# Kernel optimization log

Hardware: AMD Instinct MI355X
Metric: run time of the kernel (lower is better)

The kernel has to match this reference:

```python
import jax, jax.numpy as jnp
import numpy as np

ALPHA = 0.2  # LeakyReLU negative slope
NEG_INF = -9e15  # matches torch's -9000000000000000.0


def setup_inputs() -> dict:
    key = jax.random.key(0)
    k1, k2, k3, k4 = jax.random.split(key, 4)
    B, T, N, F_in, D = 4, 32, 512, 128, 128
    h = jax.random.normal(k1, (B, T, N, F_in), dtype=jnp.float32)
    adj = jax.random.randint(k2, (N, N), 0, 2, dtype=jnp.int32)
    # params: W ~ Linear(in_dim, out_dim, bias=False); a ~ Linear(2*out_dim, 1, bias=False)
    W = jax.random.normal(k3, (F_in, D), dtype=jnp.float32) * 0.05
    a = jax.random.normal(k4, (2 * D,), dtype=jnp.float32) * 0.05
    return {"h": h, "adj": adj, "W": W, "a": a}


def reference(h, adj, W, a):
    # h: (B,T,N,F_in), adj: (N,N), W: (F_in,D), a: (2D,)
    D = W.shape[1]
    Wh = jnp.einsum('btnf,fd->btnd', h, W)  # (B,T,N,D)
    # a . [Wh_i ; Wh_j] == a_src . Wh_i + a_dst . Wh_j -- avoids (N,N,2D) concat
    a_src, a_dst = a[:D], a[D:]
    e_src = Wh @ a_src  # (B,T,N)
    e_dst = Wh @ a_dst  # (B,T,N)
    e = jax.nn.leaky_relu(e_src[..., :, None] + e_dst[..., None, :], ALPHA)  # (B,T,N,N)
    e = jnp.where(adj > 0, e, jnp.float32(NEG_INF))
    attention = jax.nn.softmax(e, axis=-1)  # dropout is identity at eval
    h_prime = jnp.einsum('btij,btjd->btid', attention, Wh)  # (B,T,N,D)
    return h_prime
```

## Files before the change

kernel.cpp:

```cpp
#include <hip/hip_runtime.h>
#include <math.h>

typedef __attribute__((ext_vector_type(8))) short bf16x8;
typedef __attribute__((ext_vector_type(4))) float f32x4;

#define MFMA(a, b, c) __builtin_amdgcn_mfma_f32_16x16x32_bf16(a, b, c, 0, 0, 0)

constexpr int GN = 128;
constexpr int NN = 512;
constexpr int FD = 128;
#define LOG2E 1.4426950408889634f

__device__ inline unsigned rne_top16(float x) {
    unsigned u = __float_as_uint(x);
    return u + 0x7fffu + ((u >> 16) & 1u);
}
__device__ inline unsigned pack_top16(unsigned e1, unsigned e0) {
    return __builtin_amdgcn_perm(e1, e0, 0x07060302u);
}

__global__ __launch_bounds__(1024) void gat_fused_kernel(
    const float* __restrict__ h, const float* __restrict__ a,
    const int* __restrict__ adj, const float* __restrict__ W,
    float* __restrict__ out)
{
    __shared__ __attribute__((aligned(16))) unsigned short sWh[65536];
    __shared__ __attribute__((aligned(16))) float sEsrc[NN];
    __shared__ __attribute__((aligned(16))) float sEdst[NN];

    const int bid = blockIdx.x;
    const int xcd = bid & 7, slot = bid >> 3;
    const int g  = xcd * 16 + (slot >> 1);
    const int hf = slot & 1;
    const int t = threadIdx.x, lane = t & 63, w = t >> 6;
    const int l15 = lane & 15, q8 = (lane >> 4) * 8;
    const float* hg = h + (size_t)g * NN * FD;

    #pragma unroll
    for (int rep = 0; rep < 2; ++rep) {
        const int p = rep * 1024 + t;
        const int lanep = p & 63, cn2 = p >> 6;
        const int kbase = (cn2 >> 3) * 32 + ((lanep >> 4) & 3) * 8;
        const int d = (cn2 & 7) * 16 + (lanep & 15);
        unsigned hi[8], lo[8];
        #pragma unroll
        for (int idx = 0; idx < 8; ++idx) {
            const float wv = W[(kbase + idx) * FD + d];
            const unsigned u = __float_as_uint(wv);
            hi[idx] = u;
            lo[idx] = rne_top16(wv - __uint_as_float(u & 0xffff0000u));
        }
        uint4 H4, L4;
        H4.x = pack_top16(hi[1], hi[0]); H4.y = pack_top16(hi[3], hi[2]);
        H4.z = pack_top16(hi[5], hi[4]); H4.w = pack_top16(hi[7], hi[6]);
        L4.x = pack_top16(lo[1], lo[0]); L4.y = pack_top16(lo[3], lo[2]);
        L4.z = pack_top16(lo[5], lo[4]); L4.w = pack_top16(lo[7], lo[6]);
        *(uint4*)&sWh[32768 + p * 8] = H4;
        *(uint4*)&sWh[49152 + p * 8] = L4;
    }
    __syncthreads();

    f32x4 acc1[2][8];
    #pragma unroll
    for (int mt = 0; mt < 2; ++mt)
        #pragma unroll
        for (int nb = 0; nb < 8; ++nb) acc1[mt][nb] = (f32x4){0.f, 0.f, 0.f, 0.f};

    #pragma unroll
    for (int kk = 0; kk < 4; ++kk) {
        float4 hv[4];
        #pragma unroll
        for (int mt = 0; mt < 2; ++mt) {
            const float* src = hg + (size_t)(w * 32 + mt * 16 + l15) * FD
                             + kk * 32 + q8;
            hv[2 * mt]     = *(const float4*)src;
            hv[2 * mt + 1] = *(const float4*)(src + 4);
        }
        bf16x8 ah[2], al[2];
        #pragma unroll
        for (int mt = 0; mt < 2; ++mt) {
            const float4 f0 = hv[2 * mt], f1 = hv[2 * mt + 1];
            const float xs[8] = {f0.x, f0.y, f0.z, f0.w, f1.x, f1.y, f1.z, f1.w};
            union { bf16x8 v; unsigned u[4]; } H, L;
            #pragma unroll
            for (int j = 0; j < 4; ++j) {
                const unsigned e0 = __float_as_uint(xs[2 * j]);
                const unsigned e1 = __float_as_uint(xs[2 * j + 1]);
                H.u[j] = pack_top16(e1, e0);
                const unsigned l0 = rne_top16(xs[2*j]   - __uint_as_float(e0 & 0xffff0000u));
                const unsigned l1 = rne_top16(xs[2*j+1] - __uint_as_float(e1 & 0xffff0000u));
                L.u[j] = pack_top16(l1, l0);
            }
            ah[mt] = H.v; al[mt] = L.v;
        }
        #pragma unroll
        for (int nb = 0; nb < 8; ++nb) {
            const bf16x8 bh = *(const bf16x8*)&sWh[32768 + ((kk * 8 + nb) * 64 + lane) * 8];
            const bf16x8 bl = *(const bf16x8*)&sWh[49152 + ((kk * 8 + nb) * 64 + lane) * 8];
            #pragma unroll
            for (int mt = 0; mt < 2; ++mt) {
                acc1[mt][nb] = MFMA(al[mt], bh, acc1[mt][nb]);
                acc1[mt][nb] = MFMA(ah[mt], bl, acc1[mt][nb]);
                acc1[mt][nb] = MFMA(ah[mt], bh, acc1[mt][nb]);
            }
        }
    }

    {
        float av[8], bv[8];
        #pragma unroll
        for (int nb = 0; nb < 8; ++nb) {
            av[nb] = a[nb * 16 + l15];
            bv[nb] = a[FD + nb * 16 + l15];
        }
        #pragma unroll
        for (int mt = 0; mt < 2; ++mt)
            #pragma unroll
            for (int r = 0; r < 4; ++r) {
                float ps = 0.f, pd = 0.f;
                #pragma unroll
                for (int nb = 0; nb < 8; ++nb) {
                    ps += acc1[mt][nb][r] * av[nb];
                    pd += acc1[mt][nb][r] * bv[nb];
                }
                #pragma unroll
                for (int off = 1; off <= 8; off <<= 1) {
                    ps += __shfl_xor(ps, off);
                    pd += __shfl_xor(pd, off);
                }
                if (l15 == 0) {
                    const int row = w * 32 + mt * 16 + (lane >> 4) * 4 + r;
                    sEsrc[row] = ps * LOG2E;
                    sEdst[row] = pd * LOG2E;
                }
            }
    }
    __syncthreads();

    {
        const int ib = 4 * ((lane >> 4) & 1);
        #pragma unroll
        for (int mt = 0; mt < 2; ++mt) {
            const int lp2 = l15 + 16 * (mt * 2 + (lane >> 5));
            #pragma unroll
            for (int nb = 0; nb < 8; ++nb) {
                const int off = ((w * 8 + nb) * 64 + lp2) * 8 + ib;
                const unsigned r0 = rne_top16(acc1[mt][nb][0]);
                const unsigned r1 = rne_top16(acc1[mt][nb][1]);
                const unsigned r2 = rne_top16(acc1[mt][nb][2]);
                const unsigned r3 = rne_top16(acc1[mt][nb][3]);
                *(uint2*)&sWh[off] = make_uint2(pack_top16(r1, r0), pack_top16(r3, r2));
            }
        }
    }
    __syncthreads();

    const int rg = w >> 1, jh = w & 1;
    const int rloc0 = rg * 32 + l15;
    const int irow0 = hf * 256 + rloc0;
    const int irow1 = irow0 + 16;
    const float s0 = sEsrc[irow0];
    const float s1 = sEsrc[irow1];
    const int* adjr0 = adj + (size_t)irow0 * NN;
    const int* adjr1 = adj + (size_t)irow1 * NN;

    union { bf16x8 v; unsigned short s[8]; } bo;
    {
        const unsigned short oneb = (l15 == 0) ? (unsigned short)0x3f80 : (unsigned short)0;
        #pragma unroll
        for (int j = 0; j < 8; ++j) bo.s[j] = oneb;
    }

    f32x4 acc[2][8];
    #pragma unroll
    for (int mt = 0; mt < 2; ++mt)
        #pragma unroll
        for (int nb = 0; nb < 8; ++nb) acc[mt][nb] = (f32x4){0.f, 0.f, 0.f, 0.f};
    f32x4 accS0 = (f32x4){0.f, 0.f, 0.f, 0.f};
    f32x4 accS1 = (f32x4){0.f, 0.f, 0.f, 0.f};

    const int k0 = jh * 8;
    int4 n00 = *(const int4*)&adjr0[k0 * 32 + q8];
    int4 n01 = *(const int4*)&adjr0[k0 * 32 + q8 + 4];
    int4 n10 = *(const int4*)&adjr1[k0 * 32 + q8];
    int4 n11 = *(const int4*)&adjr1[k0 * 32 + q8 + 4];

    for (int kl = 0; kl < 8; ++kl) {
        const int KK = k0 + kl;
        const int4 m00 = n00, m01 = n01, m10 = n10, m11 = n11;
        if (kl < 7) {
            const int jb = (KK + 1) * 32 + q8;
            n00 = *(const int4*)&adjr0[jb];
            n01 = *(const int4*)&adjr0[jb + 4];
            n10 = *(const int4*)&adjr1[jb];
            n11 = *(const int4*)&adjr1[jb + 4];
        }
        const float* ep = &sEdst[KK * 32 + q8];
        const float4 ed0 = *(const float4*)ep;
        const float4 ed1 = *(const float4*)(ep + 4);
        const float ev[8] = {ed0.x, ed0.y, ed0.z, ed0.w, ed1.x, ed1.y, ed1.z, ed1.w};
        int ma0[8], ma1[8];
        *(int4*)&ma0[0] = m00; *(int4*)&ma0[4] = m01;
        *(int4*)&ma1[0] = m10; *(int4*)&ma1[4] = m11;

        union { bf16x8 v; unsigned u[4]; } H0, H1;
        unsigned uh0[8], uh1[8];
        #pragma unroll
        for (int i = 0; i < 8; ++i) {
            const float z0 = s0 + ev[i];
            float p0 = __builtin_amdgcn_exp2f(fmaxf(z0, 0.2f * z0));
            p0 = (ma0[i] > 0) ? p0 : 0.f;
            uh0[i] = __float_as_uint(p0);
            const float z1 = s1 + ev[i];
            float p1 = __builtin_amdgcn_exp2f(fmaxf(z1, 0.2f * z1));
            p1 = (ma1[i] > 0) ? p1 : 0.f;
            uh1[i] = __float_as_uint(p1);
        }
        #pragma unroll
        for (int j = 0; j < 4; ++j) {
            H0.u[j] = pack_top16(uh0[2*j+1], uh0[2*j]);
            H1.u[j] = pack_top16(uh1[2*j+1], uh1[2*j]);
        }
        #pragma unroll
        for (int nb = 0; nb < 8; ++nb) {
            const bf16x8 bh = *(const bf16x8*)&sWh[((KK * 8 + nb) * 64 + lane) * 8];
            acc[0][nb] = MFMA(H0.v, bh, acc[0][nb]);
            acc[1][nb] = MFMA(H1.v, bh, acc[1][nb]);
        }
        accS0 = MFMA(H0.v, bo.v, accS0);
        accS1 = MFMA(H1.v, bo.v, accS1);
    }

    __syncthreads();

    float* sPartF = (float*)sWh;
    if (jh == 1) {
        #pragma unroll
        for (int mt = 0; mt < 2; ++mt)
            #pragma unroll
            for (int nb = 0; nb < 8; ++nb)
                *(f32x4*)&sPartF[(((rg * 2 + mt) * 8 + nb) * 64 + lane) * 4] = acc[mt][nb];
        if (l15 == 0) {
            #pragma unroll
            for (int r = 0; r < 4; ++r) {
                sEsrc[rg * 32 + (lane >> 4) * 4 + r]      = accS0[r];
                sEsrc[rg * 32 + 16 + (lane >> 4) * 4 + r] = accS1[r];
            }
        }
    }
    __syncthreads();

    if (jh == 0) {
        #pragma unroll
        for (int mt = 0; mt < 2; ++mt)
            #pragma unroll
            for (int nb = 0; nb < 8; ++nb) {
                const f32x4 p = *(const f32x4*)&sPartF[(((rg * 2 + mt) * 8 + nb) * 64 + lane) * 4];
                acc[mt][nb][0] += p[0]; acc[mt][nb][1] += p[1];
                acc[mt][nb][2] += p[2]; acc[mt][nb][3] += p[3];
            }
        #pragma unroll
        for (int r = 0; r < 4; ++r) {
            const float rl0 = 1.0f / (__shfl(accS0[r], lane & 48)
                                      + sEsrc[rg * 32 + (lane >> 4) * 4 + r]);
            const float rl1 = 1.0f / (__shfl(accS1[r], lane & 48)
                                      + sEsrc[rg * 32 + 16 + (lane >> 4) * 4 + r]);
            const int row0 = g * NN + hf * 256 + rg * 32 + (lane >> 4) * 4 + r;
            const int row1 = row0 + 16;
            #pragma unroll
            for (int nb = 0; nb < 8; ++nb) {
                out[row0 * FD + nb * 16 + l15] = acc[0][nb][r] * rl0;
                out[row1 * FD + nb * 16 + l15] = acc[1][nb][r] * rl1;
            }
        }
    }
}

extern "C" void kernel_launch(void* const* d_in, const int* in_sizes, int n_in,
                              void* d_out, int out_size, void* d_ws, size_t ws_size,
                              hipStream_t stream) {
    const float* h   = (const float*)d_in[0];
    const int*   adj = (const int*)d_in[1];
    const float* W   = (const float*)d_in[2];
    const float* a   = (const float*)d_in[3];
    float* out = (float*)d_out;
    (void)d_ws; (void)ws_size;

    gat_fused_kernel<<<256, 1024, 0, stream>>>(h, a, adj, W, out);
}
```

Baseline: 116.9 us.

## Bit-pack adjacency in LDS, prefetch inputs early, software-pipeline P with MFMA

The adjacency rows for the block's 256 rows are loaded once at kernel start and packed into bitmasks in LDS, replacing per-iteration global int4 loads in the attention loop. The first h tile and the W values are issued early so their latency overlaps the mask packing. The attention loop now computes the next probability tile while the current tile's MFMAs run, and raises wave priority around the MFMA block. The final cross-wave reduction is split so each half-wave writes out one row-tile instead of one half doing all the writes. In exchange this adds LDS usage (about 17KB for the mask), more registers for the double-buffered P tiles, and a redundant expression in the s0 load.

```diff
diff --git a/kernel.cpp b/kernel.cpp
--- a/kernel.cpp
+++ b/kernel.cpp
@@ -25,6 +25,7 @@
     float* __restrict__ out)
 {
     __shared__ __attribute__((aligned(16))) unsigned short sWh[65536];
+    __shared__ unsigned maskS[4352];
     __shared__ __attribute__((aligned(16))) float sEsrc[NN];
     __shared__ __attribute__((aligned(16))) float sEdst[NN];
 
@@ -36,19 +37,54 @@
     const int l15 = lane & 15, q8 = (lane >> 4) * 8;
     const float* hg = h + (size_t)g * NN * FD;
 
+    float4 hv0[4];
+    #pragma unroll
+    for (int mt = 0; mt < 2; ++mt) {
+        const float* src = hg + (size_t)(w * 32 + mt * 16 + l15) * FD + q8;
+        hv0[2 * mt]     = *(const float4*)src;
+        hv0[2 * mt + 1] = *(const float4*)(src + 4);
+    }
+
+    float wv[16];
+    {
+        #pragma unroll
+        for (int rep = 0; rep < 2; ++rep) {
+            const int p = rep * 1024 + t;
+            const int lanep = p & 63, cn2 = p >> 6;
+            const int kbase = (cn2 >> 3) * 32 + ((lanep >> 4) & 3) * 8;
+            const int d = (cn2 & 7) * 16 + (lanep & 15);
+            #pragma unroll
+            for (int idx = 0; idx < 8; ++idx)
+                wv[rep * 8 + idx] = W[(kbase + idx) * FD + d];
+        }
+    }
+
+    #pragma unroll
+    for (int q = 0; q < 4; ++q) {
+        const int wi = t * 4 + q;
+        const int row = wi >> 4, wo = wi & 15;
+        const int* p = adj + (size_t)(hf * 256 + row) * NN + wo * 32;
+        unsigned m = 0;
+        #pragma unroll
+        for (int b = 0; b < 32; b += 4) {
+            const int4 v = *(const int4*)&p[b];
+            m |= (v.x > 0 ? 1u : 0u) << b;
+            m |= (v.y > 0 ? 1u : 0u) << (b + 1);
+            m |= (v.z > 0 ? 1u : 0u) << (b + 2);
+            m |= (v.w > 0 ? 1u : 0u) << (b + 3);
+        }
+        maskS[row * 17 + wo] = m;
+    }
+
     #pragma unroll
     for (int rep = 0; rep < 2; ++rep) {
         const int p = rep * 1024 + t;
-        const int lanep = p & 63, cn2 = p >> 6;
-        const int kbase = (cn2 >> 3) * 32 + ((lanep >> 4) & 3) * 8;
-        const int d = (cn2 & 7) * 16 + (lanep & 15);
         unsigned hi[8], lo[8];
         #pragma unroll
         for (int idx = 0; idx < 8; ++idx) {
-            const float wv = W[(kbase + idx) * FD + d];
-            const unsigned u = __float_as_uint(wv);
+            const unsigned u = __float_as_uint(wv[rep * 8 + idx]);
             hi[idx] = u;
-            lo[idx] = rne_top16(wv - __uint_as_float(u & 0xffff0000u));
+            lo[idx] = rne_top16(wv[rep * 8 + idx] - __uint_as_float(u & 0xffff0000u));
         }
         uint4 H4, L4;
         H4.x = pack_top16(hi[1], hi[0]); H4.y = pack_top16(hi[3], hi[2]);
@@ -69,12 +105,17 @@
     #pragma unroll
     for (int kk = 0; kk < 4; ++kk) {
         float4 hv[4];
-        #pragma unroll
-        for (int mt = 0; mt < 2; ++mt) {
-            const float* src = hg + (size_t)(w * 32 + mt * 16 + l15) * FD
-                             + kk * 32 + q8;
-            hv[2 * mt]     = *(const float4*)src;
-            hv[2 * mt + 1] = *(const float4*)(src + 4);
+        if (kk == 0) {
+            #pragma unroll
+            for (int q = 0; q < 4; ++q) hv[q] = hv0[q];
+        } else {
+            #pragma unroll
+            for (int mt = 0; mt < 2; ++mt) {
+                const float* src = hg + (size_t)(w * 32 + mt * 16 + l15) * FD
+                                 + kk * 32 + q8;
+                hv[2 * mt]     = *(const float4*)src;
+                hv[2 * mt + 1] = *(const float4*)(src + 4);
+            }
         }
         bf16x8 ah[2], al[2];
         #pragma unroll
@@ -157,12 +198,9 @@
 
     const int rg = w >> 1, jh = w & 1;
     const int rloc0 = rg * 32 + l15;
-    const int irow0 = hf * 256 + rloc0;
-    const int irow1 = irow0 + 16;
-    const float s0 = sEsrc[irow0];
-    const float s1 = sEsrc[irow1];
-    const int* adjr0 = adj + (size_t)irow0 * NN;
-    const int* adjr1 = adj + (size_t)irow1 * NN;
+    const int rloc1 = rloc0 + 16;
+    const float s0 = sEsrc[hf * 256 + rloc0 - 0 + (hf ? 0 : 0)] * 0.f + sEsrc[hf * 256 + rloc0];
+    const float s1 = sEsrc[hf * 256 + rloc1];
 
     union { bf16x8 v; unsigned short s[8]; } bo;
     {
@@ -179,41 +217,26 @@
     f32x4 accS0 = (f32x4){0.f, 0.f, 0.f, 0.f};
     f32x4 accS1 = (f32x4){0.f, 0.f, 0.f, 0.f};
 
-    const int k0 = jh * 8;
-    int4 n00 = *(const int4*)&adjr0[k0 * 32 + q8];
-    int4 n01 = *(const int4*)&adjr0[k0 * 32 + q8 + 4];
-    int4 n10 = *(const int4*)&adjr1[k0 * 32 + q8];
-    int4 n11 = *(const int4*)&adjr1[k0 * 32 + q8 + 4];
-
-    for (int kl = 0; kl < 8; ++kl) {
-        const int KK = k0 + kl;
-        const int4 m00 = n00, m01 = n01, m10 = n10, m11 = n11;
-        if (kl < 7) {
-            const int jb = (KK + 1) * 32 + q8;
-            n00 = *(const int4*)&adjr0[jb];
-            n01 = *(const int4*)&adjr0[jb + 4];
-            n10 = *(const int4*)&adjr1[jb];
-            n11 = *(const int4*)&adjr1[jb + 4];
-        }
+    union PU { bf16x8 v; unsigned u[4]; };
+    PU H0a, H1a, H0b, H1b;
+
+    auto computeP = [&](const int KK, PU& H0, PU& H1) {
+        const unsigned mw0 = maskS[rloc0 * 17 + KK] >> q8;
+        const unsigned mw1 = maskS[rloc1 * 17 + KK] >> q8;
         const float* ep = &sEdst[KK * 32 + q8];
         const float4 ed0 = *(const float4*)ep;
         const float4 ed1 = *(const float4*)(ep + 4);
         const float ev[8] = {ed0.x, ed0.y, ed0.z, ed0.w, ed1.x, ed1.y, ed1.z, ed1.w};
-        int ma0[8], ma1[8];
-        *(int4*)&ma0[0] = m00; *(int4*)&ma0[4] = m01;
-        *(int4*)&ma1[0] = m10; *(int4*)&ma1[4] = m11;
-
-        union { bf16x8 v; unsigned u[4]; } H0, H1;
         unsigned uh0[8], uh1[8];
         #pragma unroll
         for (int i = 0; i < 8; ++i) {
             const float z0 = s0 + ev[i];
             float p0 = __builtin_amdgcn_exp2f(fmaxf(z0, 0.2f * z0));
-            p0 = (ma0[i] > 0) ? p0 : 0.f;
+            p0 = ((mw0 >> i) & 1u) ? p0 : 0.f;
             uh0[i] = __float_as_uint(p0);
             const float z1 = s1 + ev[i];
             float p1 = __builtin_amdgcn_exp2f(fmaxf(z1, 0.2f * z1));
-            p1 = (ma1[i] > 0) ? p1 : 0.f;
+            p1 = ((mw1 >> i) & 1u) ? p1 : 0.f;
             uh1[i] = __float_as_uint(p1);
         }
         #pragma unroll
@@ -221,57 +244,87 @@
             H0.u[j] = pack_top16(uh0[2*j+1], uh0[2*j]);
             H1.u[j] = pack_top16(uh1[2*j+1], uh1[2*j]);
         }
+    };
+
+    const int k0 = jh * 8;
+    computeP(k0, H0a, H1a);
+
+    #pragma unroll
+    for (int kl = 0; kl < 8; ++kl) {
+        const int KK = k0 + kl;
+        PU& H0c = (kl & 1) ? H0b : H0a;
+        PU& H1c = (kl & 1) ? H1b : H1a;
+        PU& H0n = (kl & 1) ? H0a : H0b;
+        PU& H1n = (kl & 1) ? H1a : H1b;
+        if (kl < 7) computeP(KK + 1, H0n, H1n);
+
+        __builtin_amdgcn_s_setprio(1);
         #pragma unroll
         for (int nb = 0; nb < 8; ++nb) {
             const bf16x8 bh = *(const bf16x8*)&sWh[((KK * 8 + nb) * 64 + lane) * 8];
-            acc[0][nb] = MFMA(H0.v, bh, acc[0][nb]);
-            acc[1][nb] = MFMA(H1.v, bh, acc[1][nb]);
-        }
-        accS0 = MFMA(H0.v, bo.v, accS0);
-        accS1 = MFMA(H1.v, bo.v, accS1);
+            acc[0][nb] = MFMA(H0c.v, bh, acc[0][nb]);
+            acc[1][nb] = MFMA(H1c.v, bh, acc[1][nb]);
+        }
+        accS0 = MFMA(H0c.v, bo.v, accS0);
+        accS1 = MFMA(H1c.v, bo.v, accS1);
+        __builtin_amdgcn_s_setprio(0);
     }
 
     __syncthreads();
 
     float* sPartF = (float*)sWh;
-    if (jh == 1) {
-        #pragma unroll
-        for (int mt = 0; mt < 2; ++mt)
+    if (jh == 0) {
+        #pragma unroll
+        for (int nb = 0; nb < 8; ++nb)
+            *(f32x4*)&sPartF[(((rg * 2 + 1) * 8 + nb) * 64 + lane) * 4] = acc[1][nb];
+        if (l15 == 0) {
+            #pragma unroll
+            for (int r = 0; r < 4; ++r)
+                sEsrc[rg * 32 + 16 + (lane >> 4) * 4 + r] = accS1[r];
+        }
+    } else {
+        #pragma unroll
+        for (int nb = 0; nb < 8; ++nb)
+            *(f32x4*)&sPartF[(((rg * 2 + 0) * 8 + nb) * 64 + lane) * 4] = acc[0][nb];
+        if (l15 == 0) {
+            #pragma unroll
+            for (int r = 0; r < 4; ++r)
+                sEsrc[rg * 32 + (lane >> 4) * 4 + r] = accS0[r];
+        }
+    }
+    __syncthreads();
+
+    if (jh == 0) {
+        #pragma unroll
+        for (int nb = 0; nb < 8; ++nb) {
+            const f32x4 p = *(const f32x4*)&sPartF[(((rg * 2 + 0) * 8 + nb) * 64 + lane) * 4];
+            acc[0][nb][0] += p[0]; acc[0][nb][1] += p[1];
+            acc[0][nb][2] += p[2]; acc[0][nb][3] += p[3];
+        }
+        #pragma unroll
+        for (int r = 0; r < 4; ++r) {
+            const float rl = 1.0f / (__shfl(accS0[r], lane & 48)
+                                     + sEsrc[rg * 32 + (lane >> 4) * 4 + r]);
+            const int row = g * NN + hf * 256 + rg * 32 + (lane >> 4) * 4 + r;
             #pragma unroll
             for (int nb = 0; nb < 8; ++nb)
-                *(f32x4*)&sPartF[(((rg * 2 + mt) * 8 + nb) * 64 + lane) * 4] = acc[mt][nb];
-        if (l15 == 0) {
-            #pragma unroll
-            for (int r = 0; r < 4; ++r) {
-                sEsrc[rg * 32 + (lane >> 4) * 4 + r]      = accS0[r];
-                sEsrc[rg * 32 + 16 + (lane >> 4) * 4 + r] = accS1[r];
-            }
-        }
-    }
-    __syncthreads();
-
-    if (jh == 0) {
-        #pragma unroll
-        for (int mt = 0; mt < 2; ++mt)
-            #pragma unroll
-            for (int nb = 0; nb < 8; ++nb) {
-                const f32x4 p = *(const f32x4*)&sPartF[(((rg * 2 + mt) * 8 + nb) * 64 + lane) * 4];
-                acc[mt][nb][0] += p[0]; acc[mt][nb][1] += p[1];
-                acc[mt][nb][2] += p[2]; acc[mt][nb][3] += p[3];
-            }
+                out[row * FD + nb * 16 + l15] = acc[0][nb][r] * rl;
+        }
+    } else {
+        #pragma unroll
+        for (int nb = 0; nb < 8; ++nb) {
+            const f32x4 p = *(const f32x4*)&sPartF[(((rg * 2 + 1) * 8 + nb) * 64 + lane) * 4];
+            acc[1][nb][0] += p[0]; acc[1][nb][1] += p[1];
+            acc[1][nb][2] += p[2]; acc[1][nb][3] += p[3];
+        }
         #pragma unroll
         for (int r = 0; r < 4; ++r) {
-            const float rl0 = 1.0f / (__shfl(accS0[r], lane & 48)
-                                      + sEsrc[rg * 32 + (lane >> 4) * 4 + r]);
-            const float rl1 = 1.0f / (__shfl(accS1[r], lane & 48)
-                                      + sEsrc[rg * 32 + 16 + (lane >> 4) * 4 + r]);
-            const int row0 = g * NN + hf * 256 + rg * 32 + (lane >> 4) * 4 + r;
-            const int row1 = row0 + 16;
-            #pragma unroll
-            for (int nb = 0; nb < 8; ++nb) {
-                out[row0 * FD + nb * 16 + l15] = acc[0][nb][r] * rl0;
-                out[row1 * FD + nb * 16 + l15] = acc[1][nb][r] * rl1;
-            }
+            const float rl = 1.0f / (__shfl(accS1[r], lane & 48)
+                                     + sEsrc[rg * 32 + 16 + (lane >> 4) * 4 + r]);
+            const int row = g * NN + hf * 256 + rg * 32 + 16 + (lane >> 4) * 4 + r;
+            #pragma unroll
+            for (int nb = 0; nb < 8; ++nb)
+                out[row * FD + nb * 16 + l15] = acc[1][nb][r] * rl;
         }
     }
 }
```

New measurement: 130.4 us. +11.5%, slower.
